# Optimization experiments

Measured on AMD Instinct MI355X. Metric: run time of the kernel, lower is better.

The kernel has to match this reference:

```python
import jax, jax.numpy as jnp
import numpy as np

N_HEADS = 8
EPS = 1e-5


def setup_inputs() -> dict:
    key = jax.random.key(0)
    ks = jax.random.split(key, 5)
    B, C, H, W = 4, 512, 64, 64
    X = jax.random.normal(ks[0], (B, C, H, W), dtype=jnp.float32)
    gamma = jnp.ones((C,), dtype=jnp.float32)
    beta = jnp.zeros((C,), dtype=jnp.float32)
    Wqkv = jax.random.normal(ks[1], (3 * C, C), dtype=jnp.float32) * 0.02
    bqkv = jnp.zeros((3 * C,), dtype=jnp.float32)
    Wproj = jax.random.normal(ks[2], (C, C), dtype=jnp.float32) * 0.02
    bproj = jnp.zeros((C,), dtype=jnp.float32)
    return {"X": X, "gamma": gamma, "beta": beta, "Wqkv": Wqkv, "bqkv": bqkv,
            "Wproj": Wproj, "bproj": bproj}


def reference(X, gamma, beta, Wqkv, bqkv, Wproj, bproj):
    B, C, H, W = X.shape
    hw = H * W
    d3 = (3 * C) // N_HEADS  # 3*d_head per-head latent (QKV interleaved per head)
    scale = jnp.sqrt(jnp.asarray(C / N_HEADS, dtype=X.dtype))
    # (B, C, H, W) -> (B, hw, C)
    t = X.reshape(B, C, hw).transpose(0, 2, 1)
    # LayerNorm over channels
    mu = jnp.mean(t, axis=-1, keepdims=True)
    var = jnp.var(t, axis=-1, keepdims=True)
    t = (t - mu) * jax.lax.rsqrt(var + EPS) * gamma + beta
    # qkv linear: (B, hw, 3C)
    t = t @ Wqkv.T + bqkv
    # einops 'batch hw (heads latent) -> (batch heads) hw latent'
    t = t.reshape(B, hw, N_HEADS, d3).transpose(0, 2, 1, 3)  # (B, heads, hw, 3*d_head)
    Q, K, V = jnp.split(t, 3, axis=-1)  # each (B, heads, hw, d_head)
    S = jnp.einsum('bhqd,bhkd->bhqk', Q, K) / scale
    A = jax.nn.softmax(S, axis=-1)
    O = jnp.einsum('bhqk,bhkd->bhqd', A, V)  # (B, heads, hw, d_head)
    O = O.transpose(0, 2, 1, 3).reshape(B, hw, C)
    O = O @ Wproj.T + bproj
    return O.transpose(0, 2, 1).reshape(B, C, H, W)
```

## Files before the change

### kernel.cpp

```cpp
#include <hip/hip_runtime.h>
#include <hip/hip_bf16.h>

typedef __bf16 bf16_t;
typedef __attribute__((ext_vector_type(8))) __bf16 bf16x8;
typedef __attribute__((ext_vector_type(4))) __bf16 bf16x4;
typedef __attribute__((ext_vector_type(4))) float f32x4;

#define MFMA16(A, B, C) __builtin_amdgcn_mfma_f32_16x16x32_bf16((A), (B), (C), 0, 0, 0)

__global__ __launch_bounds__(256) void cvt_kernel(const float* __restrict__ Wq,
                                                  const float* __restrict__ Wp,
                                                  bf16_t* __restrict__ qh,
                                                  bf16_t* __restrict__ ql,
                                                  bf16_t* __restrict__ ph,
                                                  bf16_t* __restrict__ pl) {
  const int i = (blockIdx.x * 256 + threadIdx.x) * 4;
  if (i < 786432) {
    const float4 v = *(const float4*)(Wq + i);
    const float vv[4] = {v.x, v.y, v.z, v.w};
    bf16x4 h, l;
    #pragma unroll
    for (int j = 0; j < 4; ++j) {
      h[j] = (bf16_t)vv[j];
      l[j] = (bf16_t)(vv[j] - (float)h[j]);
    }
    *(bf16x4*)(qh + i) = h;
    *(bf16x4*)(ql + i) = l;
  } else {
    const int j0 = i - 786432;
    const float4 v = *(const float4*)(Wp + j0);
    const float vv[4] = {v.x, v.y, v.z, v.w};
    bf16x4 h, l;
    #pragma unroll
    for (int j = 0; j < 4; ++j) {
      h[j] = (bf16_t)vv[j];
      l[j] = (bf16_t)(vv[j] - (float)h[j]);
    }
    *(bf16x4*)(ph + j0) = h;
    *(bf16x4*)(pl + j0) = l;
  }
}

__global__ __launch_bounds__(256) void ln_kernel(const float* __restrict__ X,
                                                 const float* __restrict__ gamma,
                                                 const float* __restrict__ beta,
                                                 bf16_t* __restrict__ Th,
                                                 bf16_t* __restrict__ Tl) {
  __shared__ __align__(16) bf16_t tile[512 * 32];
  __shared__ float red1[8][32];
  __shared__ float red2[8][32];
  __shared__ float smu[32], srs[32];
  __shared__ float sg[512], sb[512];
  const int tid = threadIdx.x;
  const int g = tid >> 5, pi = tid & 31;
  const int b = blockIdx.y;
  const int p0 = blockIdx.x * 32;
  sg[tid] = gamma[tid];
  sg[tid + 256] = gamma[tid + 256];
  sb[tid] = beta[tid];
  sb[tid + 256] = beta[tid + 256];
  const float* Xb = X + ((size_t)b * 512) * 4096 + p0;
  float s1 = 0.f, s2 = 0.f;
  #pragma unroll 4
  for (int c = g * 64; c < g * 64 + 64; ++c) {
    const float x = Xb[(size_t)c * 4096 + pi];
    tile[c * 32 + pi] = (bf16_t)x;
    s1 += x;
    s2 += x * x;
  }
  red1[g][pi] = s1;
  red2[g][pi] = s2;
  __syncthreads();
  if (tid < 32) {
    float a = 0.f, q = 0.f;
    #pragma unroll
    for (int k = 0; k < 8; ++k) {
      a += red1[k][tid];
      q += red2[k][tid];
    }
    const float mu = a * (1.f / 512.f);
    const float var = q * (1.f / 512.f) - mu * mu;
    smu[tid] = mu;
    srs[tid] = rsqrtf(var + 1e-5f);
  }
  __syncthreads();
  const int pi2 = tid >> 3, qq = tid & 7;
  const float mu = smu[pi2], rs = srs[pi2];
  const size_t outoff = ((size_t)(b * 4096 + p0 + pi2)) * 512;
  #pragma unroll
  for (int ii = 0; ii < 8; ++ii) {
    const int c0 = qq * 64 + ii * 8;
    bf16x8 ph, pl;
    #pragma unroll
    for (int j = 0; j < 8; ++j) {
      const float x = (float)tile[(c0 + j) * 32 + pi2];
      const float y = (x - mu) * rs * sg[c0 + j] + sb[c0 + j];
      const bf16_t hi = (bf16_t)y;
      ph[j] = hi;
      pl[j] = (bf16_t)(y - (float)hi);
    }
    *(bf16x8*)(Th + outoff + c0) = ph;
    *(bf16x8*)(Tl + outoff + c0) = pl;
  }
}

__global__ __launch_bounds__(256) void gemm_qkv(const bf16_t* __restrict__ Wqh,
                                                const bf16_t* __restrict__ Wql,
                                                const bf16_t* __restrict__ Th,
                                                const bf16_t* __restrict__ Tl,
                                                const float* __restrict__ bqkv,
                                                bf16_t* __restrict__ QKV) {
  extern __shared__ char smem[];
  char* const Ah = smem;
  char* const Al = smem + 16384;
  char* const Bh = smem + 32768;
  char* const Bl = smem + 49152;
  const int pos0 = blockIdx.x * 128;
  const int oc0 = blockIdx.y * 128;
  const int tid = threadIdx.x;
  const int l = tid & 63, w = tid >> 6;
  const int wr = w >> 1, wc = w & 1;
  f32x4 acc[4][4] = {};
  for (int kt = 0; kt < 512; kt += 64) {
    __syncthreads();
    #pragma unroll
    for (int i = 0; i < 4; ++i) {
      const int chunk = tid + 256 * i;
      const int row = chunk >> 3, cp = chunk & 7;
      const int dst = row * 128 + ((cp * 16) ^ ((row & 7) << 4));
      const size_t offA = (size_t)(oc0 + row) * 512 + kt + cp * 8;
      const size_t offB = (size_t)(pos0 + row) * 512 + kt + cp * 8;
      *(bf16x8*)(Ah + dst) = *(const bf16x8*)(Wqh + offA);
      *(bf16x8*)(Al + dst) = *(const bf16x8*)(Wql + offA);
      *(bf16x8*)(Bh + dst) = *(const bf16x8*)(Th + offB);
      *(bf16x8*)(Bl + dst) = *(const bf16x8*)(Tl + offB);
    }
    __syncthreads();
    #pragma unroll
    for (int ks = 0; ks < 2; ++ks) {
      bf16x8 ah[4], al[4], bh[4], bl[4];
      #pragma unroll
      for (int mt = 0; mt < 4; ++mt) {
        const int row = wr * 64 + mt * 16 + (l & 15);
        const int off = row * 128 + ((ks * 64 + (l >> 4) * 16) ^ ((row & 7) << 4));
        ah[mt] = *(const bf16x8*)(Ah + off);
        al[mt] = *(const bf16x8*)(Al + off);
      }
      #pragma unroll
      for (int nt = 0; nt < 4; ++nt) {
        const int row = wc * 64 + nt * 16 + (l & 15);
        const int off = row * 128 + ((ks * 64 + (l >> 4) * 16) ^ ((row & 7) << 4));
        bh[nt] = *(const bf16x8*)(Bh + off);
        bl[nt] = *(const bf16x8*)(Bl + off);
      }
      #pragma unroll
      for (int mt = 0; mt < 4; ++mt)
        #pragma unroll
        for (int nt = 0; nt < 4; ++nt) {
          acc[mt][nt] = MFMA16(ah[mt], bh[nt], acc[mt][nt]);
          acc[mt][nt] = MFMA16(ah[mt], bl[nt], acc[mt][nt]);
          acc[mt][nt] = MFMA16(al[mt], bh[nt], acc[mt][nt]);
        }
    }
  }
  #pragma unroll
  for (int mt = 0; mt < 4; ++mt) {
    const int ocb = oc0 + wr * 64 + mt * 16 + 4 * (l >> 4);
    const float4 bias = *(const float4*)(bqkv + ocb);
    #pragma unroll
    for (int nt = 0; nt < 4; ++nt) {
      const int pos = pos0 + wc * 64 + nt * 16 + (l & 15);
      bf16x4 o;
      o[0] = (bf16_t)(acc[mt][nt][0] + bias.x);
      o[1] = (bf16_t)(acc[mt][nt][1] + bias.y);
      o[2] = (bf16_t)(acc[mt][nt][2] + bias.z);
      o[3] = (bf16_t)(acc[mt][nt][3] + bias.w);
      *(bf16x4*)(QKV + (size_t)pos * 1536 + ocb) = o;
    }
  }
}

__global__ __launch_bounds__(256) void attn_kernel(const bf16_t* __restrict__ QKV,
                                                   bf16_t* __restrict__ Oh,
                                                   bf16_t* __restrict__ Ol) {
  const int o = blockIdx.x;
  const int sid = (o & 7) * 128 + (o >> 3);
  const int qt = sid & 31;
  const int bh = sid >> 5;
  const int b = bh >> 3, h = bh & 7;
  const int tid = threadIdx.x;
  const int l = tid & 63, w = tid >> 6;
  const int lg = l >> 4, lr = l & 15;

  __shared__ __align__(16) bf16_t KsA[64 * 64];
  __shared__ __align__(16) bf16_t KsB[64 * 64];
  __shared__ __align__(16) bf16_t Vt[64 * 72];
  __shared__ __align__(16) bf16_t Ps[4][32 * 64];
  __shared__ float Lred[4][32];

  const bf16_t* base = QKV + (size_t)(b * 4096) * 1536 + h * 192;
  const bf16_t* kbase = base + 64;
  const bf16_t* vbase = base + 128;
  const int q0 = qt * 128 + w * 32;

  bf16x8 qf[2][2];
  #pragma unroll
  for (int mq = 0; mq < 2; ++mq)
    #pragma unroll
    for (int ks = 0; ks < 2; ++ks) {
      bf16x8 v = *(const bf16x8*)(base + (size_t)(q0 + mq * 16 + lr) * 1536 +
                                  ks * 32 + 8 * lg);
      #pragma unroll
      for (int j = 0; j < 8; ++j) v[j] = (bf16_t)(0.125f * (float)v[j]);
      qf[mq][ks] = v;
    }

  f32x4 acc_o[2][4] = {};
  float lsum[2] = {0.f, 0.f};
  char* const psw = (char*)&Ps[w][0];

  auto stageK = [&](bf16_t* dst, int k0) {
    #pragma unroll
    for (int i = 0; i < 2; ++i) {
      const int c = tid + 256 * i;
      const int row = c >> 3;
      const int cp = (c & 7) ^ (row & 7);
      const bf16_t* g = kbase + (size_t)(k0 + row) * 1536 + cp * 8;
      __builtin_amdgcn_global_load_lds(
          (const __attribute__((address_space(1))) void*)g,
          (__attribute__((address_space(3))) void*)((char*)dst + c * 16), 16, 0, 0);
    }
  };
  auto loadV = [&](int k0, bf16x8& v0, bf16x8& v1) {
    const bf16_t* vs = vbase + (size_t)(k0 + l) * 1536 + w * 16;
    v0 = *(const bf16x8*)vs;
    v1 = *(const bf16x8*)(vs + 8);
  };
  auto writeV = [&](bf16x8 v0, bf16x8 v1) {
    #pragma unroll
    for (int j = 0; j < 8; ++j) {
      Vt[(w * 16 + j) * 72 + l] = v0[j];
      Vt[(w * 16 + 8 + j) * 72 + l] = v1[j];
    }
  };
  auto compute = [&](const bf16_t* Kbuf) {
    f32x4 st[4][2] = {};
    __builtin_amdgcn_s_setprio(1);
    #pragma unroll
    for (int ks = 0; ks < 2; ++ks) {
      bf16x8 kb[4];
      #pragma unroll
      for (int kt = 0; kt < 4; ++kt) {
        const int row = kt * 16 + lr;
        kb[kt] = *(const bf16x8*)((const char*)Kbuf + row * 128 +
                                  ((ks * 64 + lg * 16) ^ ((row & 7) << 4)));
      }
      #pragma unroll
      for (int kt = 0; kt < 4; ++kt) {
        st[kt][0] = MFMA16(kb[kt], qf[0][ks], st[kt][0]);
        st[kt][1] = MFMA16(kb[kt], qf[1][ks], st[kt][1]);
      }
    }
    __builtin_amdgcn_s_setprio(0);
    #pragma unroll
    for (int mq = 0; mq < 2; ++mq) {
      const int prow = mq * 16 + lr;
      const int rs = (prow & 7) << 4;
      #pragma unroll
      for (int kt = 0; kt < 4; ++kt) {
        const float p0 = __expf(st[kt][mq][0]);
        const float p1 = __expf(st[kt][mq][1]);
        const float p2 = __expf(st[kt][mq][2]);
        const float p3 = __expf(st[kt][mq][3]);
        lsum[mq] += (p0 + p1) + (p2 + p3);
        bf16x4 pk;
        pk[0] = (bf16_t)p0;
        pk[1] = (bf16_t)p1;
        pk[2] = (bf16_t)p2;
        pk[3] = (bf16_t)p3;
        *(bf16x4*)(psw + prow * 128 + ((kt * 32 + lg * 8) ^ rs)) = pk;
      }
    }
    #pragma unroll
    for (int ks = 0; ks < 2; ++ks) {
      bf16x8 pa[2], vb[4];
      #pragma unroll
      for (int mt = 0; mt < 2; ++mt) {
        const int row = mt * 16 + lr;
        pa[mt] = *(const bf16x8*)(psw + row * 128 +
                                  ((ks * 64 + lg * 16) ^ ((row & 7) << 4)));
      }
      #pragma unroll
      for (int dt = 0; dt < 4; ++dt)
        vb[dt] = *(const bf16x8*)((const char*)Vt + (dt * 16 + lr) * 144 +
                                  ks * 64 + lg * 16);
      __builtin_amdgcn_s_setprio(1);
      #pragma unroll
      for (int mt = 0; mt < 2; ++mt)
        #pragma unroll
        for (int dt = 0; dt < 4; ++dt)
          acc_o[mt][dt] = MFMA16(pa[mt], vb[dt], acc_o[mt][dt]);
      __builtin_amdgcn_s_setprio(0);
    }
  };

  stageK(KsA, 0);
  bf16x8 va0, va1, vb0, vb1;
  loadV(0, va0, va1);

  for (int t = 0; t < 64; t += 2) {
    __syncthreads();
    writeV(va0, va1);
    __syncthreads();
    stageK(KsB, (t + 1) * 64);
    loadV((t + 1) * 64, vb0, vb1);
    compute(KsA);

    __syncthreads();
    writeV(vb0, vb1);
    __syncthreads();
    if (t + 2 < 64) {
      stageK(KsA, (t + 2) * 64);
      loadV((t + 2) * 64, va0, va1);
    }
    compute(KsB);
  }

  lsum[0] += __shfl_xor(lsum[0], 16);
  lsum[0] += __shfl_xor(lsum[0], 32);
  lsum[1] += __shfl_xor(lsum[1], 16);
  lsum[1] += __shfl_xor(lsum[1], 32);
  if (lg == 0) {
    Lred[w][lr] = lsum[0];
    Lred[w][16 + lr] = lsum[1];
  }
  __syncthreads();

  #pragma unroll
  for (int mt = 0; mt < 2; ++mt) {
    #pragma unroll
    for (int r = 0; r < 4; ++r) {
      const int row = mt * 16 + 4 * lg + r;
      const float inv = 1.f / Lred[w][row];
      const int rsw = (row & 7) << 4;
      #pragma unroll
      for (int dt = 0; dt < 4; ++dt) {
        const float v = acc_o[mt][dt][r] * inv;
        acc_o[mt][dt][r] = v;
        const int col = dt * 16 + lr;
        *(bf16_t*)(psw + ((row * 128 + col * 2) ^ rsw)) = (bf16_t)v;
      }
    }
  }
  const int row2 = l & 31, hf = l >> 5;
  {
    bf16_t* orow = Oh + (size_t)(b * 4096 + q0 + row2) * 512 + h * 64 + hf * 32;
    #pragma unroll
    for (int c = 0; c < 4; ++c) {
      const bf16x8 vv =
          *(const bf16x8*)(psw + ((row2 * 128 + hf * 64 + c * 16) ^ ((row2 & 7) << 4)));
      *(bf16x8*)(orow + c * 8) = vv;
    }
  }
  #pragma unroll
  for (int mt = 0; mt < 2; ++mt) {
    #pragma unroll
    for (int r = 0; r < 4; ++r) {
      const int row = mt * 16 + 4 * lg + r;
      const int rsw = (row & 7) << 4;
      #pragma unroll
      for (int dt = 0; dt < 4; ++dt) {
        const float v = acc_o[mt][dt][r];
        const bf16_t hi = (bf16_t)v;
        const bf16_t lo = (bf16_t)(v - (float)hi);
        const int col = dt * 16 + lr;
        *(bf16_t*)(psw + ((row * 128 + col * 2) ^ rsw)) = lo;
      }
    }
  }
  {
    bf16_t* orow = Ol + (size_t)(b * 4096 + q0 + row2) * 512 + h * 64 + hf * 32;
    #pragma unroll
    for (int c = 0; c < 4; ++c) {
      const bf16x8 vv =
          *(const bf16x8*)(psw + ((row2 * 128 + hf * 64 + c * 16) ^ ((row2 & 7) << 4)));
      *(bf16x8*)(orow + c * 8) = vv;
    }
  }
}

__global__ __launch_bounds__(256) void gemm_proj(const bf16_t* __restrict__ Oh,
                                                 const bf16_t* __restrict__ Ol,
                                                 const bf16_t* __restrict__ Wph,
                                                 const bf16_t* __restrict__ Wpl,
                                                 const float* __restrict__ bproj,
                                                 float* __restrict__ Y) {
  extern __shared__ char smem[];
  char* const Ah = smem;
  char* const Al = smem + 16384;
  char* const Bh = smem + 32768;
  char* const Bl = smem + 49152;
  const int pos0 = blockIdx.y * 128;
  const int oc0 = blockIdx.x * 128;
  const int tid = threadIdx.x;
  const int l = tid & 63, w = tid >> 6;
  const int wr = w >> 1, wc = w & 1;
  f32x4 acc[4][4] = {};
  for (int kt = 0; kt < 512; kt += 64) {
    __syncthreads();
    #pragma unroll
    for (int i = 0; i < 4; ++i) {
      const int chunk = tid + 256 * i;
      const int row = chunk >> 3, cp = chunk & 7;
      const int dst = row * 128 + ((cp * 16) ^ ((row & 7) << 4));
      const size_t offA = (size_t)(pos0 + row) * 512 + kt + cp * 8;
      const size_t offB = (size_t)(oc0 + row) * 512 + kt + cp * 8;
      *(bf16x8*)(Ah + dst) = *(const bf16x8*)(Oh + offA);
      *(bf16x8*)(Al + dst) = *(const bf16x8*)(Ol + offA);
      *(bf16x8*)(Bh + dst) = *(const bf16x8*)(Wph + offB);
      *(bf16x8*)(Bl + dst) = *(const bf16x8*)(Wpl + offB);
    }
    __syncthreads();
    #pragma unroll
    for (int ks = 0; ks < 2; ++ks) {
      bf16x8 ah[4], al[4], bh[4], bl[4];
      #pragma unroll
      for (int mt = 0; mt < 4; ++mt) {
        const int row = wr * 64 + mt * 16 + (l & 15);
        const int off = row * 128 + ((ks * 64 + (l >> 4) * 16) ^ ((row & 7) << 4));
        ah[mt] = *(const bf16x8*)(Ah + off);
        al[mt] = *(const bf16x8*)(Al + off);
      }
      #pragma unroll
      for (int nt = 0; nt < 4; ++nt) {
        const int row = wc * 64 + nt * 16 + (l & 15);
        const int off = row * 128 + ((ks * 64 + (l >> 4) * 16) ^ ((row & 7) << 4));
        bh[nt] = *(const bf16x8*)(Bh + off);
        bl[nt] = *(const bf16x8*)(Bl + off);
      }
      #pragma unroll
      for (int mt = 0; mt < 4; ++mt)
        #pragma unroll
        for (int nt = 0; nt < 4; ++nt) {
          acc[mt][nt] = MFMA16(ah[mt], bh[nt], acc[mt][nt]);
          acc[mt][nt] = MFMA16(ah[mt], bl[nt], acc[mt][nt]);
          acc[mt][nt] = MFMA16(al[mt], bh[nt], acc[mt][nt]);
        }
    }
  }
  #pragma unroll
  for (int mt = 0; mt < 4; ++mt) {
    const int posb = pos0 + wr * 64 + mt * 16 + 4 * (l >> 4);
    const int bb_ = posb >> 12, p = posb & 4095;
    #pragma unroll
    for (int nt = 0; nt < 4; ++nt) {
      const int oc = oc0 + wc * 64 + nt * 16 + (l & 15);
      const float bias = bproj[oc];
      float4 v;
      v.x = acc[mt][nt][0] + bias;
      v.y = acc[mt][nt][1] + bias;
      v.z = acc[mt][nt][2] + bias;
      v.w = acc[mt][nt][3] + bias;
      *(float4*)(Y + ((size_t)(bb_ * 512 + oc)) * 4096 + p) = v;
    }
  }
}

extern "C" void kernel_launch(void* const* d_in, const int* in_sizes, int n_in,
                              void* d_out, int out_size, void* d_ws, size_t ws_size,
                              hipStream_t stream) {
  const float* X = (const float*)d_in[0];
  const float* gamma = (const float*)d_in[1];
  const float* beta = (const float*)d_in[2];
  const float* Wqkv = (const float*)d_in[3];
  const float* bqkv = (const float*)d_in[4];
  const float* Wproj = (const float*)d_in[5];
  const float* bproj = (const float*)d_in[6];
  float* Y = (float*)d_out;
  char* ws = (char*)d_ws;

  bf16_t* Wq_hi = (bf16_t*)(ws + 0);
  bf16_t* Wq_lo = (bf16_t*)(ws + 1572864);
  bf16_t* Wp_hi = (bf16_t*)(ws + 3145728);
  bf16_t* Wp_lo = (bf16_t*)(ws + 3670016);
  bf16_t* T_hi = (bf16_t*)(ws + 4194304);
  bf16_t* T_lo = (bf16_t*)(ws + 20971520);
  bf16_t* QKVb = (bf16_t*)(ws + 37748736);
  bf16_t* O_hi = T_hi;
  bf16_t* O_lo = T_lo;

  cvt_kernel<<<1024, 256, 0, stream>>>(Wqkv, Wproj, Wq_hi, Wq_lo, Wp_hi, Wp_lo);
  ln_kernel<<<dim3(128, 4), 256, 0, stream>>>(X, gamma, beta, T_hi, T_lo);
  gemm_qkv<<<dim3(128, 12), 256, 65536, stream>>>(Wq_hi, Wq_lo, T_hi, T_lo, bqkv, QKVb);
  attn_kernel<<<dim3(1024), 256, 0, stream>>>(QKVb, O_hi, O_lo);
  gemm_proj<<<dim3(4, 128), 256, 65536, stream>>>(O_hi, O_lo, Wp_hi, Wp_lo, bproj, Y);
}
```

Before: 427.8 us.

## Use direct global-to-LDS loads in GEMMs and streamline attention softmax

Both GEMM kernels now stage tiles with global_load_lds, so data goes straight into swizzled LDS and no longer passes through registers. The QKV GEMM epilogue folds the softmax scale and log2(e) into Q, which lets attention use exp2 directly and drops the per-element Q rescale. Row sums are now computed by an MFMA against a ones vector instead of shuffles and an LDS reduction, the V transpose buffer is XOR-swizzled instead of padded, and attention gets an occupancy hint in its launch bounds. The risks are the extra MFMA work, possible register pressure from the occupancy target, and unchanged unbounded exp with no max subtraction.

```diff
diff --git a/kernel.cpp b/kernel.cpp
--- a/kernel.cpp
+++ b/kernel.cpp
@@ -7,6 +7,14 @@
 typedef __attribute__((ext_vector_type(4))) float f32x4;
 
 #define MFMA16(A, B, C) __builtin_amdgcn_mfma_f32_16x16x32_bf16((A), (B), (C), 0, 0, 0)
+
+#if __has_builtin(__builtin_amdgcn_exp2f)
+#define EXP2F(x) __builtin_amdgcn_exp2f(x)
+#else
+#define EXP2F(x) exp2f(x)
+#endif
+
+#define QSCALE 0.1803368801111244f
 
 __global__ __launch_bounds__(256) void cvt_kernel(const float* __restrict__ Wq,
                                                   const float* __restrict__ Wp,
@@ -126,14 +134,22 @@
     #pragma unroll
     for (int i = 0; i < 4; ++i) {
       const int chunk = tid + 256 * i;
-      const int row = chunk >> 3, cp = chunk & 7;
-      const int dst = row * 128 + ((cp * 16) ^ ((row & 7) << 4));
+      const int row = chunk >> 3;
+      const int cp = (chunk & 7) ^ (row & 7);
       const size_t offA = (size_t)(oc0 + row) * 512 + kt + cp * 8;
       const size_t offB = (size_t)(pos0 + row) * 512 + kt + cp * 8;
-      *(bf16x8*)(Ah + dst) = *(const bf16x8*)(Wqh + offA);
-      *(bf16x8*)(Al + dst) = *(const bf16x8*)(Wql + offA);
-      *(bf16x8*)(Bh + dst) = *(const bf16x8*)(Th + offB);
-      *(bf16x8*)(Bl + dst) = *(const bf16x8*)(Tl + offB);
+      __builtin_amdgcn_global_load_lds(
+          (const __attribute__((address_space(1))) void*)(Wqh + offA),
+          (__attribute__((address_space(3))) void*)(Ah + chunk * 16), 16, 0, 0);
+      __builtin_amdgcn_global_load_lds(
+          (const __attribute__((address_space(1))) void*)(Wql + offA),
+          (__attribute__((address_space(3))) void*)(Al + chunk * 16), 16, 0, 0);
+      __builtin_amdgcn_global_load_lds(
+          (const __attribute__((address_space(1))) void*)(Th + offB),
+          (__attribute__((address_space(3))) void*)(Bh + chunk * 16), 16, 0, 0);
+      __builtin_amdgcn_global_load_lds(
+          (const __attribute__((address_space(1))) void*)(Tl + offB),
+          (__attribute__((address_space(3))) void*)(Bl + chunk * 16), 16, 0, 0);
     }
     __syncthreads();
     #pragma unroll
@@ -167,22 +183,23 @@
   for (int mt = 0; mt < 4; ++mt) {
     const int ocb = oc0 + wr * 64 + mt * 16 + 4 * (l >> 4);
     const float4 bias = *(const float4*)(bqkv + ocb);
+    const float qs = ((ocb % 192) < 64) ? QSCALE : 1.0f;
     #pragma unroll
     for (int nt = 0; nt < 4; ++nt) {
       const int pos = pos0 + wc * 64 + nt * 16 + (l & 15);
       bf16x4 o;
-      o[0] = (bf16_t)(acc[mt][nt][0] + bias.x);
-      o[1] = (bf16_t)(acc[mt][nt][1] + bias.y);
-      o[2] = (bf16_t)(acc[mt][nt][2] + bias.z);
-      o[3] = (bf16_t)(acc[mt][nt][3] + bias.w);
+      o[0] = (bf16_t)((acc[mt][nt][0] + bias.x) * qs);
+      o[1] = (bf16_t)((acc[mt][nt][1] + bias.y) * qs);
+      o[2] = (bf16_t)((acc[mt][nt][2] + bias.z) * qs);
+      o[3] = (bf16_t)((acc[mt][nt][3] + bias.w) * qs);
       *(bf16x4*)(QKV + (size_t)pos * 1536 + ocb) = o;
     }
   }
 }
 
-__global__ __launch_bounds__(256) void attn_kernel(const bf16_t* __restrict__ QKV,
-                                                   bf16_t* __restrict__ Oh,
-                                                   bf16_t* __restrict__ Ol) {
+__global__ __launch_bounds__(256, 4) void attn_kernel(const bf16_t* __restrict__ QKV,
+                                                      bf16_t* __restrict__ Oh,
+                                                      bf16_t* __restrict__ Ol) {
   const int o = blockIdx.x;
   const int sid = (o & 7) * 128 + (o >> 3);
   const int qt = sid & 31;
@@ -194,9 +211,8 @@
 
   __shared__ __align__(16) bf16_t KsA[64 * 64];
   __shared__ __align__(16) bf16_t KsB[64 * 64];
-  __shared__ __align__(16) bf16_t Vt[64 * 72];
+  __shared__ __align__(16) bf16_t Vt[64 * 64];
   __shared__ __align__(16) bf16_t Ps[4][32 * 64];
-  __shared__ float Lred[4][32];
 
   const bf16_t* base = QKV + (size_t)(b * 4096) * 1536 + h * 192;
   const bf16_t* kbase = base + 64;
@@ -207,16 +223,19 @@
   #pragma unroll
   for (int mq = 0; mq < 2; ++mq)
     #pragma unroll
-    for (int ks = 0; ks < 2; ++ks) {
-      bf16x8 v = *(const bf16x8*)(base + (size_t)(q0 + mq * 16 + lr) * 1536 +
-                                  ks * 32 + 8 * lg);
-      #pragma unroll
-      for (int j = 0; j < 8; ++j) v[j] = (bf16_t)(0.125f * (float)v[j]);
-      qf[mq][ks] = v;
-    }
+    for (int ks = 0; ks < 2; ++ks)
+      qf[mq][ks] = *(const bf16x8*)(base + (size_t)(q0 + mq * 16 + lr) * 1536 +
+                                    ks * 32 + 8 * lg);
+
+  bf16x8 onesb;
+  {
+    const bf16_t one = (bf16_t)1.0f;
+    #pragma unroll
+    for (int j = 0; j < 8; ++j) onesb[j] = one;
+  }
 
   f32x4 acc_o[2][4] = {};
-  float lsum[2] = {0.f, 0.f};
+  f32x4 acc_d[2] = {};
   char* const psw = (char*)&Ps[w][0];
 
   auto stageK = [&](bf16_t* dst, int k0) {
@@ -237,10 +256,12 @@
     v1 = *(const bf16x8*)(vs + 8);
   };
   auto writeV = [&](bf16x8 v0, bf16x8 v1) {
+    char* const vt = (char*)Vt;
     #pragma unroll
     for (int j = 0; j < 8; ++j) {
-      Vt[(w * 16 + j) * 72 + l] = v0[j];
-      Vt[(w * 16 + 8 + j) * 72 + l] = v1[j];
+      const int d0 = w * 16 + j, d1 = w * 16 + 8 + j;
+      *(bf16_t*)(vt + d0 * 128 + ((2 * l) ^ ((d0 & 7) << 4))) = v0[j];
+      *(bf16_t*)(vt + d1 * 128 + ((2 * l) ^ ((d1 & 7) << 4))) = v1[j];
     }
   };
   auto compute = [&](const bf16_t* Kbuf) {
@@ -268,16 +289,11 @@
       const int rs = (prow & 7) << 4;
       #pragma unroll
       for (int kt = 0; kt < 4; ++kt) {
-        const float p0 = __expf(st[kt][mq][0]);
-        const float p1 = __expf(st[kt][mq][1]);
-        const float p2 = __expf(st[kt][mq][2]);
-        const float p3 = __expf(st[kt][mq][3]);
-        lsum[mq] += (p0 + p1) + (p2 + p3);
         bf16x4 pk;
-        pk[0] = (bf16_t)p0;
-        pk[1] = (bf16_t)p1;
-        pk[2] = (bf16_t)p2;
-        pk[3] = (bf16_t)p3;
+        pk[0] = (bf16_t)EXP2F(st[kt][mq][0]);
+        pk[1] = (bf16_t)EXP2F(st[kt][mq][1]);
+        pk[2] = (bf16_t)EXP2F(st[kt][mq][2]);
+        pk[3] = (bf16_t)EXP2F(st[kt][mq][3]);
         *(bf16x4*)(psw + prow * 128 + ((kt * 32 + lg * 8) ^ rs)) = pk;
       }
     }
@@ -291,15 +307,19 @@
                                   ((ks * 64 + lg * 16) ^ ((row & 7) << 4)));
       }
       #pragma unroll
-      for (int dt = 0; dt < 4; ++dt)
-        vb[dt] = *(const bf16x8*)((const char*)Vt + (dt * 16 + lr) * 144 +
-                                  ks * 64 + lg * 16);
+      for (int dt = 0; dt < 4; ++dt) {
+        const int row = dt * 16 + lr;
+        vb[dt] = *(const bf16x8*)((const char*)Vt + row * 128 +
+                                  ((ks * 64 + lg * 16) ^ ((row & 7) << 4)));
+      }
       __builtin_amdgcn_s_setprio(1);
       #pragma unroll
-      for (int mt = 0; mt < 2; ++mt)
+      for (int mt = 0; mt < 2; ++mt) {
         #pragma unroll
         for (int dt = 0; dt < 4; ++dt)
           acc_o[mt][dt] = MFMA16(pa[mt], vb[dt], acc_o[mt][dt]);
+        acc_d[mt] = MFMA16(pa[mt], onesb, acc_d[mt]);
+      }
       __builtin_amdgcn_s_setprio(0);
     }
   };
@@ -326,22 +346,12 @@
     compute(KsB);
   }
 
-  lsum[0] += __shfl_xor(lsum[0], 16);
-  lsum[0] += __shfl_xor(lsum[0], 32);
-  lsum[1] += __shfl_xor(lsum[1], 16);
-  lsum[1] += __shfl_xor(lsum[1], 32);
-  if (lg == 0) {
-    Lred[w][lr] = lsum[0];
-    Lred[w][16 + lr] = lsum[1];
-  }
-  __syncthreads();
-
   #pragma unroll
   for (int mt = 0; mt < 2; ++mt) {
     #pragma unroll
     for (int r = 0; r < 4; ++r) {
+      const float inv = 1.f / acc_d[mt][r];
       const int row = mt * 16 + 4 * lg + r;
-      const float inv = 1.f / Lred[w][row];
       const int rsw = (row & 7) << 4;
       #pragma unroll
       for (int dt = 0; dt < 4; ++dt) {
@@ -411,14 +421,22 @@
     #pragma unroll
     for (int i = 0; i < 4; ++i) {
       const int chunk = tid + 256 * i;
-      const int row = chunk >> 3, cp = chunk & 7;
-      const int dst = row * 128 + ((cp * 16) ^ ((row & 7) << 4));
+      const int row = chunk >> 3;
+      const int cp = (chunk & 7) ^ (row & 7);
       const size_t offA = (size_t)(pos0 + row) * 512 + kt + cp * 8;
       const size_t offB = (size_t)(oc0 + row) * 512 + kt + cp * 8;
-      *(bf16x8*)(Ah + dst) = *(const bf16x8*)(Oh + offA);
-      *(bf16x8*)(Al + dst) = *(const bf16x8*)(Ol + offA);
-      *(bf16x8*)(Bh + dst) = *(const bf16x8*)(Wph + offB);
-      *(bf16x8*)(Bl + dst) = *(const bf16x8*)(Wpl + offB);
+      __builtin_amdgcn_global_load_lds(
+          (const __attribute__((address_space(1))) void*)(Oh + offA),
+          (__attribute__((address_space(3))) void*)(Ah + chunk * 16), 16, 0, 0);
+      __builtin_amdgcn_global_load_lds(
+          (const __attribute__((address_space(1))) void*)(Ol + offA),
+          (__attribute__((address_space(3))) void*)(Al + chunk * 16), 16, 0, 0);
+      __builtin_amdgcn_global_load_lds(
+          (const __attribute__((address_space(1))) void*)(Wph + offB),
+          (__attribute__((address_space(3))) void*)(Bh + chunk * 16), 16, 0, 0);
+      __builtin_amdgcn_global_load_lds(
+          (const __attribute__((address_space(1))) void*)(Wpl + offB),
+          (__attribute__((address_space(3))) void*)(Bl + chunk * 16), 16, 0, 0);
     }
     __syncthreads();
     #pragma unroll
```

New measurement: 532.4 us. 1.24x slower.
